# Optimization experiments

Hardware: AMD Instinct MI355X
Metric: run time of the kernel (lower is better)

## Reference

```python
import jax, jax.numpy as jnp
import numpy as np
from jax.scipy.special import logsumexp

NUM_JOINT_TYPES = 17
SINKHORN_ITERS = 30
SINKHORN_TAU = 0.05
BIG_COST = 1.0e6


def _scot_forward(embeddings, W1, b1, prototype_pool, joint_types, k):
    n = embeddings.shape[0]
    # node encoder: Linear + SELU
    h = jax.nn.selu(embeddings @ W1 + b1)  # [N, H]
    prototypes = prototype_pool[:k]        # [K, H] (k <= k_max)
    # squared euclidean distance (torch.cdist(p=2).pow(2))
    d2 = (jnp.sum(h * h, axis=1)[:, None]
          + jnp.sum(prototypes * prototypes, axis=1)[None, :]
          - 2.0 * (h @ prototypes.T))
    d2 = jnp.maximum(d2, 0.0)              # [N, K]
    # expand each person slot to 17 joint-type slots
    cost = jnp.repeat(d2, NUM_JOINT_TYPES, axis=1)          # [N, K*17]
    slot_types = jnp.tile(jnp.arange(NUM_JOINT_TYPES), k)   # [K*17]
    type_mask = joint_types[:, None] == slot_types[None, :]  # [N, K*17]
    cost = jnp.where(type_mask, cost, BIG_COST)

    n_slots = k * NUM_JOINT_TYPES
    log_K = -cost / SINKHORN_TAU
    log_K_ext = jnp.concatenate([log_K, jnp.zeros((n, 1), log_K.dtype)], axis=1)  # [N, K*17+1]
    # target marginal: 1 per slot, slack column absorbs leftover mass
    tm = jnp.ones(n_slots + 1, log_K.dtype).at[-1].set(float(max(n - n_slots, 1)))
    log_tm = jnp.log(tm)

    def step(carry, _):
        log_u, log_v = carry
        log_u = -logsumexp(log_K_ext + log_v[None, :], axis=1)   # row normalization
        log_v = log_tm - logsumexp(log_K_ext + log_u[:, None], axis=0)  # col normalization
        return (log_u, log_v), None

    init = (jnp.zeros(n, log_K.dtype), jnp.zeros(n_slots + 1, log_K.dtype))
    (log_u, log_v), _ = jax.lax.scan(step, init, None, length=SINKHORN_ITERS)

    T = jnp.exp(log_K_ext + log_u[:, None] + log_v[None, :])[:, :n_slots]  # [N, K*17]
    logits = jnp.log(T.reshape(n, k, NUM_JOINT_TYPES).sum(axis=2) + 1e-8)  # [N, K]
    return logits, T


def setup_inputs() -> dict:
    key = jax.random.key(0)
    k_emb, k_w, k_proto, k_jt = jax.random.split(key, 4)
    N, D, H, KMAX = 6144, 256, 256, 512
    emb = jax.random.normal(k_emb, (N, D), dtype=jnp.float32)
    emb = emb / jnp.linalg.norm(emb, axis=1, keepdims=True)  # L2-normalised per docstring
    W1 = jax.random.normal(k_w, (D, H), dtype=jnp.float32) * (1.0 / np.sqrt(D))
    b1 = jnp.zeros((H,), jnp.float32)
    prototype_pool = jax.random.normal(k_proto, (KMAX, H), dtype=jnp.float32) * 0.5
    joint_types = jax.random.randint(k_jt, (N,), 0, NUM_JOINT_TYPES)
    return {"embeddings": emb, "W1": W1, "b1": b1,
            "prototype_pool": prototype_pool, "joint_types": joint_types, "k": 300}


def reference(embeddings, W1, b1, prototype_pool, joint_types, k):
    return _scot_forward(embeddings, W1, b1, prototype_pool, joint_types, k)
```

## Files before the change

kernel.cpp:

```cpp
#include <hip/hip_runtime.h>
#include <math.h>

#define NT 17
#define NBLK 34
#define KCAP 300
#define KP 320
#define LROW 656
#define LCAP 200
#define CH 2
#define NITER 30
#define NCHKMAX 512
#define MSCALE2 28.853900817779268f

typedef unsigned long long u64;
typedef float vfloat4 __attribute__((ext_vector_type(4)));

#define EX2(x) __builtin_amdgcn_exp2f(x)
#define LG2(x) __builtin_amdgcn_logf(x)
#if __has_builtin(__builtin_amdgcn_rcpf)
#define RCP(x) __builtin_amdgcn_rcpf(x)
#else
#define RCP(x) (1.0f / (x))
#endif

__device__ inline unsigned bf16rne(float x) {
  unsigned u = __float_as_uint(x);
  return (u + 0x7FFFu + ((u >> 16) & 1u)) >> 16;
}
__device__ inline unsigned bfp(float lo, float hi) {
  return bf16rne(lo) | (bf16rne(hi) << 16);
}
#define BFLO(p) __uint_as_float((p) << 16)
#define BFHI(p) __uint_as_float((p) & 0xFFFF0000u)


__device__ inline float selu_f(float x) {
  const float scale = 1.0507009873554804934193349852946f;
  const float alpha = 1.6732632423543772848170429916717f;
  return x > 0.f ? scale * x : scale * alpha * (EX2(x * 1.4426950408889634f) - 1.f);
}

__global__ __launch_bounds__(1024) void k_bucket(const int* __restrict__ jt, int n,
    int* __restrict__ meta, int* __restrict__ perm, int* __restrict__ tys,
    unsigned* __restrict__ cmE, unsigned* __restrict__ pcE,
    unsigned* __restrict__ suE) {
  __shared__ int cnt[NCHKMAX][NT];
  __shared__ int tot[NT];
  __shared__ int off[NT];
  int tid = threadIdx.x, lane = tid & 63, wv = tid >> 6;
  int nchk = (n + 63) >> 6;

  for (int i = tid; i < NBLK * 16; i += 1024) cmE[i] = 0u;
  for (int i = tid; i < 4 * NBLK * 16; i += 1024) { pcE[i] = 0u; suE[i] = 0u; }

  for (int ci = wv; ci < nchk; ci += 16) {
    int idx = ci * 64 + lane;
    bool ok = idx < n;
    int t = ok ? jt[idx] : -1;
#pragma unroll
    for (int tt = 0; tt < NT; tt++) {
      u64 b = __ballot(t == tt);
      if (lane == tt) cnt[ci][tt] = (int)__popcll(b);
    }
  }
  __syncthreads();
  if (tid < NT) {
    int run = 0;
    for (int ci = 0; ci < nchk; ci++) {
      int x = cnt[ci][tid];
      cnt[ci][tid] = run;
      run += x;
    }
    tot[tid] = run;
  }
  __syncthreads();
  if (tid == 0) {
    int o = 0;
    for (int t = 0; t < NT; t++) {
      off[t] = o; meta[32 + t] = o; meta[t] = tot[t]; o += tot[t];
    }
  }
  __syncthreads();
  if (tid < NT) {
    int o = off[tid];
    for (int ci = 0; ci < nchk; ci++) cnt[ci][tid] += o;
  }
  __syncthreads();
  for (int ci = wv; ci < nchk; ci += 16) {
    int idx = ci * 64 + lane;
    bool ok = idx < n;
    int t = ok ? jt[idx] : -1;
    u64 myb = 0;
#pragma unroll
    for (int tt = 0; tt < NT; tt++) {
      u64 b = __ballot(t == tt);
      if (t == tt) myb = b;
    }
    if (ok) {
      int rank = (int)__popcll(myb & ((1ull << lane) - 1ull));
      int pos = cnt[ci][t] + rank;
      perm[pos] = idx;
      tys[pos] = t;
    }
  }
}

__global__ __launch_bounds__(256) void k_hgemm(const float* __restrict__ A,
    const float* __restrict__ B, const float* __restrict__ bias,
    float* __restrict__ C, int n, int D, int H) {
  __shared__ __align__(16) float As[16][68];
  __shared__ __align__(16) float Bs[16][68];
  int tid = threadIdx.x;
  int i0 = blockIdx.x * 64, j0 = blockIdx.y * 64;
  int tx = tid & 15, ty = tid >> 4;
  int aI = tid & 63, aK = (tid >> 6) << 2;
  int bJ = (tid & 15) << 2, bK = tid >> 4;
  float acc[4][4] = {};
  for (int k0 = 0; k0 < D; k0 += 16) {
    float4 av = *(const float4*)(A + (size_t)(i0 + aI) * D + k0 + aK);
    float4 bv = *(const float4*)(B + (size_t)(k0 + bK) * H + j0 + bJ);
    __syncthreads();
    As[aK + 0][aI] = av.x; As[aK + 1][aI] = av.y; As[aK + 2][aI] = av.z; As[aK + 3][aI] = av.w;
    *(float4*)(&Bs[bK][bJ]) = bv;
    __syncthreads();
#pragma unroll
    for (int kk = 0; kk < 16; kk++) {
      float4 a4 = *(float4*)(&As[kk][ty << 2]);
      float4 b4 = *(float4*)(&Bs[kk][tx << 2]);
      float aa[4] = {a4.x, a4.y, a4.z, a4.w};
      float bb[4] = {b4.x, b4.y, b4.z, b4.w};
#pragma unroll
      for (int p = 0; p < 4; p++)
#pragma unroll
        for (int q = 0; q < 4; q++)
          acc[p][q] = fmaf(aa[p], bb[q], acc[p][q]);
    }
  }
#pragma unroll
  for (int p = 0; p < 4; p++) {
    int i = i0 + (ty << 2) + p;
    float o[4];
#pragma unroll
    for (int q = 0; q < 4; q++) {
      int j = j0 + (tx << 2) + q;
      o[q] = selu_f(acc[p][q] + bias[j]);
    }
    *(float4*)(C + (size_t)i * H + j0 + (tx << 2)) = make_float4(o[0], o[1], o[2], o[3]);
  }
}

__global__ __launch_bounds__(256) void k_msort(const float* __restrict__ h,
    const float* __restrict__ P, const int* __restrict__ perm,
    float* __restrict__ Ms, int n, int H, int k) {
  __shared__ __align__(16) float As[16][68];
  __shared__ __align__(16) float Bs[16][68];
  __shared__ float hp[4][64];
  __shared__ float pp[4][64];
  __shared__ int gIdx[64];
  int tid = threadIdx.x;
  int i0 = blockIdx.x * 64, j0 = blockIdx.y * 64;
  if (tid < 64) gIdx[tid] = perm[i0 + tid];
  __syncthreads();
  int tx = tid & 15, ty = tid >> 4;
  int aI = tid & 63, aK = (tid >> 6) << 2;
  int gA = gIdx[aI];
  bool bok = (j0 + aI) < k;
  const float* bRow = P + (size_t)(j0 + (bok ? aI : 0)) * H;
  float acc[4][4] = {};
  float ha = 0.f, pa = 0.f;
  for (int k0 = 0; k0 < H; k0 += 16) {
    float4 av = *(const float4*)(h + (size_t)gA * H + k0 + aK);
    float4 bv = *(const float4*)(bRow + k0 + aK);
    ha += av.x * av.x + av.y * av.y + av.z * av.z + av.w * av.w;
    pa += bv.x * bv.x + bv.y * bv.y + bv.z * bv.z + bv.w * bv.w;
    __syncthreads();
    As[aK + 0][aI] = av.x; As[aK + 1][aI] = av.y; As[aK + 2][aI] = av.z; As[aK + 3][aI] = av.w;
    Bs[aK + 0][aI] = bv.x; Bs[aK + 1][aI] = bv.y; Bs[aK + 2][aI] = bv.z; Bs[aK + 3][aI] = bv.w;
    __syncthreads();
#pragma unroll
    for (int kk = 0; kk < 16; kk++) {
      float4 a4 = *(float4*)(&As[kk][ty << 2]);
      float4 b4 = *(float4*)(&Bs[kk][tx << 2]);
      float aa[4] = {a4.x, a4.y, a4.z, a4.w};
      float bb[4] = {b4.x, b4.y, b4.z, b4.w};
#pragma unroll
      for (int p = 0; p < 4; p++)
#pragma unroll
        for (int q = 0; q < 4; q++)
          acc[p][q] = fmaf(aa[p], bb[q], acc[p][q]);
    }
  }
  int grp = tid >> 6;
  hp[grp][aI] = ha;
  pp[grp][aI] = pa;
  __syncthreads();
#pragma unroll
  for (int p = 0; p < 4; p++) {
    int rr = (ty << 2) + p;
    int r = i0 + rr;
    float hq = hp[0][rr] + hp[1][rr] + hp[2][rr] + hp[3][rr];
#pragma unroll
    for (int q = 0; q < 4; q++) {
      int jl = (tx << 2) + q;
      int j = j0 + jl;
      if (j < k) {
        float pq = pp[0][jl] + pp[1][jl] + pp[2][jl] + pp[3][jl];
        float d2 = hq + pq - 2.f * acc[p][q];
        d2 = fmaxf(d2, 0.f);
        Ms[(size_t)r * k + j] = -d2 * MSCALE2;
      }
    }
  }
}

__global__ __launch_bounds__(1024) void k_sink(const float* __restrict__ Ms,
    unsigned short* __restrict__ Ms2, const int* __restrict__ meta,
    float* __restrict__ cmD, unsigned* __restrict__ cmE,
    float* __restrict__ pcD, unsigned* __restrict__ pcE,
    float* __restrict__ suD, unsigned* __restrict__ suE,
    float* __restrict__ uF, float* __restrict__ vF,
    int k, float tm_last) {
  __shared__ __align__(16) char Klds[LCAP * LROW];
  __shared__ __align__(16) float WP2[16][KP];
  __shared__ __align__(16) float V[KP];
  __shared__ __align__(16) float Sown[KP];
  __shared__ float SU[16];
  __shared__ float w_sh;
  __shared__ int lvl_ep;
  __shared__ int pairflag;
  int tid = threadIdx.x, lane = tid & 63, wv = tid >> 6;
  int c = blockIdx.x;
  int t, hb, prt;
  if (c < 32) { t = c & 15; hb = c >> 4; prt = c ^ 16; }
  else        { t = 16;     hb = c & 1;  prt = c ^ 1;  }
  int cRt = meta[t];
  int s0t = meta[32 + t];
  int h0 = (cRt + 1) >> 1;
  int rb = hb ? h0 : 0;
  int re = hb ? cRt : h0;
  int myR = re - rb;
  int s0 = s0t + rb;
  int ntH = (myR + 3) >> 2;
  bool l2v = (lane + 64) < (k >> 2);
  int g = lane >> 4, cg = lane & 15;
  bool r2a = (cg < 8);

  if (tid == 0) { w_sh = 1.f; lvl_ep = 0; pairflag = 0; }

  {
    float4 cm0 = make_float4(-3e38f, -3e38f, -3e38f, -3e38f);
    float4 cm1 = cm0;
    for (int tile = wv; tile < ntH; tile += 16) {
      int r0 = tile * 4;
#pragma unroll
      for (int rr = 0; rr < 4; rr++) {
        int rc = (r0 + rr < myR) ? (r0 + rr) : r0;
        const float4* rp = (const float4*)(Ms + (size_t)(s0 + rc) * k);
        float4 a0 = rp[lane];
        cm0.x = fmaxf(cm0.x, a0.x); cm0.y = fmaxf(cm0.y, a0.y);
        cm0.z = fmaxf(cm0.z, a0.z); cm0.w = fmaxf(cm0.w, a0.w);
        if (l2v) {
          float4 a1 = rp[lane + 64];
          cm1.x = fmaxf(cm1.x, a1.x); cm1.y = fmaxf(cm1.y, a1.y);
          cm1.z = fmaxf(cm1.z, a1.z); cm1.w = fmaxf(cm1.w, a1.w);
        }
      }
    }
    *(float4*)&WP2[wv][4 * lane] = cm0;
    if (l2v) *(float4*)&WP2[wv][4 * (lane + 64)] = cm1;
    __syncthreads();
    if (tid < k) {
      float cmax = WP2[0][tid];
#pragma unroll
      for (int q = 1; q < 16; q++) cmax = fmaxf(cmax, WP2[q][tid]);
      Sown[tid] = cmax;
      __hip_atomic_store(&cmD[c * KP + tid], cmax,
                         __ATOMIC_RELAXED, __HIP_MEMORY_SCOPE_AGENT);
    }
    __syncthreads();
    if (tid == 0) {
      __hip_atomic_store(&cmE[c * 16], 1u, __ATOMIC_RELAXED, __HIP_MEMORY_SCOPE_AGENT);
      while (__hip_atomic_load(&cmE[prt * 16], __ATOMIC_RELAXED, __HIP_MEMORY_SCOPE_AGENT) < 1u)
        __builtin_amdgcn_s_sleep(1);
      __hip_atomic_store(&pairflag, 1, __ATOMIC_RELEASE, __HIP_MEMORY_SCOPE_WORKGROUP);
    }
    if (tid < k) {
      while (__hip_atomic_load(&pairflag, __ATOMIC_ACQUIRE, __HIP_MEMORY_SCOPE_WORKGROUP) < 1)
        __builtin_amdgcn_s_sleep(1);
      float o = __hip_atomic_load(&cmD[prt * KP + tid],
                                  __ATOMIC_RELAXED, __HIP_MEMORY_SCOPE_AGENT);
      V[tid] = fmaxf(Sown[tid], o);
    }
    __syncthreads();
    float4 cx0 = *(const float4*)&V[4 * lane];
    float4 cx1 = l2v ? *(const float4*)&V[4 * (lane + 64)] : cx0;
    for (int tile = wv; tile < ntH; tile += 16) {
      int r0 = tile * 4;
#pragma unroll
      for (int rr = 0; rr < 4; rr++) {
        int r = r0 + rr;
        if (r < myR) {
          const float4* rp = (const float4*)(Ms + (size_t)(s0 + r) * k);
          char* orow = (char*)Ms2 + (size_t)(s0 + r) * (KP * 2);
          char* lrow = Klds + (size_t)r * LROW;
          bool inL = (r < LCAP);
          float4 a0 = rp[lane];
          uint2 o;
          o.x = bfp(EX2(a0.x - cx0.x), EX2(a0.y - cx0.y));
          o.y = bfp(EX2(a0.z - cx0.z), EX2(a0.w - cx0.w));
          *(uint2*)(orow + 8 * lane) = o;
          if (inL) *(uint2*)(lrow + 8 * lane) = o;
          if (l2v) {
            float4 a1 = rp[lane + 64];
            uint2 o1;
            o1.x = bfp(EX2(a1.x - cx1.x), EX2(a1.y - cx1.y));
            o1.y = bfp(EX2(a1.z - cx1.z), EX2(a1.w - cx1.w));
            *(uint2*)(orow + 512 + 8 * lane) = o1;
            if (inL) *(uint2*)(lrow + 512 + 8 * lane) = o1;
          } else if (lane < 16) {
            *(uint2*)(orow + 512 + 8 * lane) = make_uint2(0u, 0u);
            if (inL) *(uint2*)(lrow + 512 + 8 * lane) = make_uint2(0u, 0u);
          }
        }
      }
    }
  }
  __syncthreads();
  if (tid < KP) V[tid] = 0.f;
  __syncthreads();

  for (int m = 0; m < NITER; m++) {
    int epoch = m + 1;
    int slot = m & 3;
    if (wv == 15) {
      if (m > 0) {
        int pslot = (m - 1) & 3;
        unsigned want = (unsigned)m;
        bool need = lane < NBLK;
        for (;;) {
          bool ok = !need ||
              (__hip_atomic_load(&suE[(pslot * NBLK + lane) * 16],
                                 __ATOMIC_RELAXED, __HIP_MEMORY_SCOPE_AGENT) >= want);
          if (__all(ok)) break;
          __builtin_amdgcn_s_sleep(1);
        }
        float s = need
            ? __hip_atomic_load(&suD[(pslot * NBLK + lane) * 16],
                                __ATOMIC_RELAXED, __HIP_MEMORY_SCOPE_AGENT)
            : 0.f;
#pragma unroll
        for (int o = 32; o; o >>= 1) s += __shfl_xor(s, o);
        if (lane == 0) w_sh = tm_last / s;
      }
      if (lane == 0)
        __hip_atomic_store(&lvl_ep, epoch, __ATOMIC_RELEASE, __HIP_MEMORY_SCOPE_WORKGROUP);
    }
    float w = 0.f;
    bool haveW = (wv == 15);
    float su = 0.f;
    float vv[3][8];
#pragma unroll
    for (int q3 = 0; q3 < 3; q3++) {
      if (q3 < 2 || r2a) {
        float4 x0 = *(const float4*)&V[q3 * 128 + cg * 8];
        float4 x1 = *(const float4*)&V[q3 * 128 + cg * 8 + 4];
        vv[q3][0] = x0.x; vv[q3][1] = x0.y; vv[q3][2] = x0.z; vv[q3][3] = x0.w;
        vv[q3][4] = x1.x; vv[q3][5] = x1.y; vv[q3][6] = x1.z; vv[q3][7] = x1.w;
      } else {
#pragma unroll
        for (int e = 0; e < 8; e++) vv[q3][e] = 0.f;
      }
    }
    float acc[3][8];
#pragma unroll
    for (int q3 = 0; q3 < 3; q3++)
#pragma unroll
      for (int e = 0; e < 8; e++) acc[q3][e] = 0.f;

    int t0 = (wv < 15) ? wv : ntH;
    for (; t0 < ntH; t0 += 15 * CH) {
      uint4 T[CH][3];
      float rs[CH];
#pragma unroll
      for (int ccc = 0; ccc < CH; ccc++) {
        int tile = t0 + 15 * ccc;
        rs[ccc] = 0.f;
        if (tile < ntH) {
          int r = tile * 4 + g;
          int rc = (r < myR) ? r : (myR - 1);
          uint4 z4 = make_uint4(0u, 0u, 0u, 0u);
          if (rc < LCAP) {
            const uint4* lp = (const uint4*)(Klds + (size_t)rc * LROW + (cg << 4));
            T[ccc][0] = lp[0];
            T[ccc][1] = lp[16];
            if (r2a) T[ccc][2] = lp[32]; else T[ccc][2] = z4;
          } else {
            const uint4* gp = (const uint4*)((const char*)Ms2 +
                (size_t)(s0 + rc) * (KP * 2) + (cg << 4));
            T[ccc][0] = gp[0];
            T[ccc][1] = gp[16];
            if (r2a) T[ccc][2] = gp[32]; else T[ccc][2] = z4;
          }
          float r1 = 0.f;
#pragma unroll
          for (int q3 = 0; q3 < 3; q3++) {
            r1 = fmaf(BFLO(T[ccc][q3].x), vv[q3][0], r1);
            r1 = fmaf(BFHI(T[ccc][q3].x), vv[q3][1], r1);
            r1 = fmaf(BFLO(T[ccc][q3].y), vv[q3][2], r1);
            r1 = fmaf(BFHI(T[ccc][q3].y), vv[q3][3], r1);
            r1 = fmaf(BFLO(T[ccc][q3].z), vv[q3][4], r1);
            r1 = fmaf(BFHI(T[ccc][q3].z), vv[q3][5], r1);
            r1 = fmaf(BFLO(T[ccc][q3].w), vv[q3][6], r1);
            r1 = fmaf(BFHI(T[ccc][q3].w), vv[q3][7], r1);
          }
          r1 += __shfl_xor(r1, 1); r1 += __shfl_xor(r1, 2);
          r1 += __shfl_xor(r1, 4); r1 += __shfl_xor(r1, 8);
          rs[ccc] = r1;
        }
      }
      if (!haveW) {
        while (__hip_atomic_load(&lvl_ep, __ATOMIC_ACQUIRE, __HIP_MEMORY_SCOPE_WORKGROUP) < epoch)
          __builtin_amdgcn_s_sleep(1);
        w = w_sh;
        haveW = true;
      }
#pragma unroll
      for (int ccc = 0; ccc < CH; ccc++) {
        int tile = t0 + 15 * ccc;
        if (tile < ntH) {
          int r = tile * 4 + g;
          bool valid = (r < myR);
          float u = RCP(rs[ccc] + w);
          float uu = valid ? u : 0.f;
          if (cg == 0) {
            su += uu;
            if (valid && m == NITER - 1) uF[s0 + r] = u;
          }
#pragma unroll
          for (int q3 = 0; q3 < 3; q3++) {
            acc[q3][0] = fmaf(BFLO(T[ccc][q3].x), uu, acc[q3][0]);
            acc[q3][1] = fmaf(BFHI(T[ccc][q3].x), uu, acc[q3][1]);
            acc[q3][2] = fmaf(BFLO(T[ccc][q3].y), uu, acc[q3][2]);
            acc[q3][3] = fmaf(BFHI(T[ccc][q3].y), uu, acc[q3][3]);
            acc[q3][4] = fmaf(BFLO(T[ccc][q3].z), uu, acc[q3][4]);
            acc[q3][5] = fmaf(BFHI(T[ccc][q3].z), uu, acc[q3][5]);
            acc[q3][6] = fmaf(BFLO(T[ccc][q3].w), uu, acc[q3][6]);
            acc[q3][7] = fmaf(BFHI(T[ccc][q3].w), uu, acc[q3][7]);
          }
        }
      }
    }
    if (!haveW) {
      while (__hip_atomic_load(&lvl_ep, __ATOMIC_ACQUIRE, __HIP_MEMORY_SCOPE_WORKGROUP) < epoch)
        __builtin_amdgcn_s_sleep(1);
      haveW = true;
    }

    if (wv < 15) {
#pragma unroll
      for (int q3 = 0; q3 < 3; q3++)
#pragma unroll
        for (int e = 0; e < 8; e++) {
          float a = acc[q3][e];
          a += __shfl_xor(a, 16);
          a += __shfl_xor(a, 32);
          acc[q3][e] = a;
        }
      if (lane < 16) {
#pragma unroll
        for (int q3 = 0; q3 < 3; q3++) {
          if (q3 < 2 || lane < 8) {
            *(float4*)&WP2[wv][q3 * 128 + lane * 8] =
                make_float4(acc[q3][0], acc[q3][1], acc[q3][2], acc[q3][3]);
            *(float4*)&WP2[wv][q3 * 128 + lane * 8 + 4] =
                make_float4(acc[q3][4], acc[q3][5], acc[q3][6], acc[q3][7]);
          }
        }
      }
      float sr = su;
      sr += __shfl_xor(sr, 16);
      sr += __shfl_xor(sr, 32);
      if (lane == 0) SU[wv] = sr;
    }
    __syncthreads();
    if (tid < k) {
      float s = WP2[0][tid];
#pragma unroll
      for (int q = 1; q < 15; q++) s += WP2[q][tid];
      Sown[tid] = s;
      __hip_atomic_store(&pcD[(slot * NBLK + c) * KP + tid], s,
                         __ATOMIC_RELAXED, __HIP_MEMORY_SCOPE_AGENT);
    }
    if (wv == 15) {
      float sp = (lane < 15) ? SU[lane] : 0.f;
#pragma unroll
      for (int o = 32; o; o >>= 1) sp += __shfl_xor(sp, o);
      if (lane == 0)
        __hip_atomic_store(&suD[(slot * NBLK + c) * 16], sp,
                           __ATOMIC_RELAXED, __HIP_MEMORY_SCOPE_AGENT);
      __builtin_amdgcn_s_waitcnt(0);
      if (lane == 0)
        __hip_atomic_store(&suE[(slot * NBLK + c) * 16], (unsigned)epoch,
                           __ATOMIC_RELAXED, __HIP_MEMORY_SCOPE_AGENT);
    }
    __syncthreads();
    if (tid == 0) {
      __hip_atomic_store(&pcE[(slot * NBLK + c) * 16], (unsigned)epoch,
                         __ATOMIC_RELAXED, __HIP_MEMORY_SCOPE_AGENT);
      while (__hip_atomic_load(&pcE[(slot * NBLK + prt) * 16],
                               __ATOMIC_RELAXED, __HIP_MEMORY_SCOPE_AGENT) < (unsigned)epoch)
        __builtin_amdgcn_s_sleep(1);
      __hip_atomic_store(&pairflag, m + 2, __ATOMIC_RELEASE, __HIP_MEMORY_SCOPE_WORKGROUP);
    }
    if (tid < k) {
      while (__hip_atomic_load(&pairflag, __ATOMIC_ACQUIRE, __HIP_MEMORY_SCOPE_WORKGROUP) < m + 2)
        __builtin_amdgcn_s_sleep(1);
      float sp = __hip_atomic_load(&pcD[(slot * NBLK + prt) * KP + tid],
                                   __ATOMIC_RELAXED, __HIP_MEMORY_SCOPE_AGENT);
      V[tid] = RCP(Sown[tid] + sp);
    }
    __syncthreads();
  }
  if (hb == 0)
    for (int j = tid; j < k; j += 1024) vF[(size_t)t * k + j] = V[j];
}

__global__ __launch_bounds__(256) void k_epi(const unsigned short* __restrict__ Ms2,
    const float* __restrict__ uF, const float* __restrict__ vF,
    const int* __restrict__ perm, const int* __restrict__ tys,
    float* __restrict__ out, int n, int k) {
  __shared__ float vals[KCAP];
  int r = blockIdx.x;
  int i = perm[r], t = tys[r];
  float u = uF[r];
  const unsigned short* Krow = Ms2 + (size_t)r * KP;
  const float* Vrow = vF + (size_t)t * k;
  for (int j = threadIdx.x; j < k; j += 256)
    vals[j] = __uint_as_float((unsigned)Krow[j] << 16) * u * Vrow[j];
  __syncthreads();
  float* lg = out + (size_t)i * k;
  for (int j = threadIdx.x; j < k; j += 256)
    __builtin_nontemporal_store(LG2(vals[j] + 1e-8f) * 0.6931471805599453f, &lg[j]);
  int ns = k * NT;
  float* Trow = out + (size_t)n * k + (size_t)i * ns;
  if ((ns & 3) == 0) {
    int n4 = ns >> 2;
    int o0 = threadIdx.x << 2;
    int rmod = o0 % NT;
    for (int g4 = threadIdx.x; g4 < n4; g4 += 256, o0 += 1024) {
      int sstar = t - rmod; if (sstar < 0) sstar += NT;
      int j = (unsigned)(o0 + sstar) / (unsigned)NT;
      float vv = vals[j < k ? j : 0];
      vfloat4 v;
      v.x = (sstar == 0) ? vv : 0.f;
      v.y = (sstar == 1) ? vv : 0.f;
      v.z = (sstar == 2) ? vv : 0.f;
      v.w = (sstar == 3) ? vv : 0.f;
      __builtin_nontemporal_store(v, (vfloat4*)(Trow + o0));
      rmod += 4; if (rmod >= NT) rmod -= NT;
    }
  } else {
    for (int o = threadIdx.x; o < ns; o += 256) {
      int j = o / NT;
      int tt = o - j * NT;
      Trow[o] = (tt == t) ? vals[j] : 0.f;
    }
  }
}

extern "C" void kernel_launch(void* const* d_in, const int* in_sizes, int n_in,
                              void* d_out, int out_size, void* d_ws, size_t ws_size,
                              hipStream_t stream) {
  const float* emb = (const float*)d_in[0];
  const float* W1  = (const float*)d_in[1];
  const float* b1  = (const float*)d_in[2];
  const float* P   = (const float*)d_in[3];
  const int*   jt  = (const int*)d_in[4];
  (void)n_in; (void)ws_size;

  const int n = in_sizes[4];
  const int H = in_sizes[2];
  const int D = in_sizes[1] / H;
  const int k = out_size / (n * (NT + 1));
  const int nslots = k * NT;
  const float tm_last = (float)((n - nslots) > 1 ? (n - nslots) : 1);

  char* w = (char*)d_ws;
  size_t off = 0;
  auto take = [&](size_t bytes) -> char* {
    char* p = w + off;
    off = (off + bytes + 255) & ~(size_t)255;
    return p;
  };
  int*      meta = (int*)take(4096);
  int*      perm = (int*)take((size_t)n * 4);
  int*      tys  = (int*)take((size_t)n * 4);
  float*    h    = (float*)take((size_t)n * H * 4);
  float*    Ms   = (float*)take((size_t)n * k * 4);
  unsigned short* Ms2 = (unsigned short*)take((size_t)n * KP * 2 + 1024);
  float*    cmD  = (float*)take((size_t)NBLK * KP * 4);
  unsigned* cmE  = (unsigned*)take((size_t)NBLK * 64);
  float*    pcD  = (float*)take((size_t)4 * NBLK * KP * 4);
  unsigned* pcE  = (unsigned*)take((size_t)4 * NBLK * 64);
  float*    suD  = (float*)take((size_t)4 * NBLK * 64);
  unsigned* suE  = (unsigned*)take((size_t)4 * NBLK * 64);
  float*    uF   = (float*)take((size_t)n * 4);
  float*    vF   = (float*)take((size_t)NT * k * 4);

  k_bucket<<<1, 1024, 0, stream>>>(jt, n, meta, perm, tys, cmE, pcE, suE);
  k_hgemm<<<dim3(n / 64, H / 64), dim3(256), 0, stream>>>(emb, W1, b1, h, n, D, H);
  k_msort<<<dim3(n / 64, (k + 63) / 64), dim3(256), 0, stream>>>(h, P, perm, Ms, n, H, k);
  k_sink<<<NBLK, 1024, 0, stream>>>(Ms, Ms2, meta, cmD, cmE, pcD, pcE,
                                    suD, suE, uF, vF, k, tm_last);
  k_epi<<<n, 256, 0, stream>>>(Ms2, uF, vF, perm, tys, (float*)d_out, n, k);
}
```

Before: 422.1 us.

## Replace pair-flag handoff with per-wave direct partner polling in Sinkhorn loop

Removes the shared-memory pairflag relay and the per-iteration tail barrier. Each compute wave now polls the partner block's epoch flag itself and computes column scalings directly from the partner's partial sums at the start of the next iteration, so the per-iteration V write and extra __syncthreads go away. The final vF is computed the same way after the loop. This trades one block-wide barrier per iteration for redundant per-wave global atomic loads and reciprocal work. Sown reuse across iterations could race if not guarded by the existing barriers.

```diff
diff --git a/kernel.cpp b/kernel.cpp
--- a/kernel.cpp
+++ b/kernel.cpp
@@ -227,7 +227,6 @@
   __shared__ float SU[16];
   __shared__ float w_sh;
   __shared__ int lvl_ep;
-  __shared__ int pairflag;
   int tid = threadIdx.x, lane = tid & 63, wv = tid >> 6;
   int c = blockIdx.x;
   int t, hb, prt;
@@ -245,7 +244,7 @@
   int g = lane >> 4, cg = lane & 15;
   bool r2a = (cg < 8);
 
-  if (tid == 0) { w_sh = 1.f; lvl_ep = 0; pairflag = 0; }
+  if (tid == 0) { w_sh = 1.f; lvl_ep = 0; }
 
   {
     float4 cm0 = make_float4(-3e38f, -3e38f, -3e38f, -3e38f);
@@ -278,14 +277,10 @@
                          __ATOMIC_RELAXED, __HIP_MEMORY_SCOPE_AGENT);
     }
     __syncthreads();
-    if (tid == 0) {
-      __hip_atomic_store(&cmE[c * 16], 1u, __ATOMIC_RELAXED, __HIP_MEMORY_SCOPE_AGENT);
-      while (__hip_atomic_load(&cmE[prt * 16], __ATOMIC_RELAXED, __HIP_MEMORY_SCOPE_AGENT) < 1u)
-        __builtin_amdgcn_s_sleep(1);
-      __hip_atomic_store(&pairflag, 1, __ATOMIC_RELEASE, __HIP_MEMORY_SCOPE_WORKGROUP);
-    }
+    if (tid == 0)
+      __hip_atomic_store(&cmE[c * 16], 1u, __ATOMIC_RELEASE, __HIP_MEMORY_SCOPE_AGENT);
     if (tid < k) {
-      while (__hip_atomic_load(&pairflag, __ATOMIC_ACQUIRE, __HIP_MEMORY_SCOPE_WORKGROUP) < 1)
+      while (__hip_atomic_load(&cmE[prt * 16], __ATOMIC_ACQUIRE, __HIP_MEMORY_SCOPE_AGENT) < 1u)
         __builtin_amdgcn_s_sleep(1);
       float o = __hip_atomic_load(&cmD[prt * KP + tid],
                                   __ATOMIC_RELAXED, __HIP_MEMORY_SCOPE_AGENT);
@@ -326,8 +321,6 @@
     }
   }
   __syncthreads();
-  if (tid < KP) V[tid] = 0.f;
-  __syncthreads();
 
   for (int m = 0; m < NITER; m++) {
     int epoch = m + 1;
@@ -360,15 +353,26 @@
     float su = 0.f;
     float vv[3][8];
 #pragma unroll
-    for (int q3 = 0; q3 < 3; q3++) {
-      if (q3 < 2 || r2a) {
-        float4 x0 = *(const float4*)&V[q3 * 128 + cg * 8];
-        float4 x1 = *(const float4*)&V[q3 * 128 + cg * 8 + 4];
-        vv[q3][0] = x0.x; vv[q3][1] = x0.y; vv[q3][2] = x0.z; vv[q3][3] = x0.w;
-        vv[q3][4] = x1.x; vv[q3][5] = x1.y; vv[q3][6] = x1.z; vv[q3][7] = x1.w;
-      } else {
-#pragma unroll
-        for (int e = 0; e < 8; e++) vv[q3][e] = 0.f;
+    for (int q3 = 0; q3 < 3; q3++)
+#pragma unroll
+      for (int e = 0; e < 8; e++) vv[q3][e] = 0.f;
+    if (wv < 15 && m > 0) {
+      int pslot = (m - 1) & 3;
+      while (__hip_atomic_load(&pcE[(pslot * NBLK + prt) * 16],
+                               __ATOMIC_ACQUIRE, __HIP_MEMORY_SCOPE_AGENT) < (unsigned)m)
+        __builtin_amdgcn_s_sleep(1);
+      const float* pd = pcD + ((size_t)pslot * NBLK + prt) * KP;
+#pragma unroll
+      for (int q3 = 0; q3 < 3; q3++) {
+#pragma unroll
+        for (int e = 0; e < 8; e++) {
+          int idx = q3 * 128 + cg * 8 + e;
+          if ((q3 < 2 || r2a) && idx < k) {
+            float sp = __hip_atomic_load(&pd[idx],
+                                         __ATOMIC_RELAXED, __HIP_MEMORY_SCOPE_AGENT);
+            vv[q3][e] = RCP(Sown[idx] + sp);
+          }
+        }
       }
     }
     float acc[3][8];
@@ -484,11 +488,15 @@
     }
     __syncthreads();
     if (tid < k) {
-      float s = WP2[0][tid];
-#pragma unroll
-      for (int q = 1; q < 15; q++) s += WP2[q][tid];
+      float sA = WP2[0][tid];
+#pragma unroll
+      for (int q = 1; q < 8; q++) sA += WP2[q][tid];
+      float sB = WP2[8][tid];
+#pragma unroll
+      for (int q = 9; q < 15; q++) sB += WP2[q][tid];
+      float s = sA + sB;
       Sown[tid] = s;
-      __hip_atomic_store(&pcD[(slot * NBLK + c) * KP + tid], s,
+      __hip_atomic_store(&pcD[((size_t)slot * NBLK + c) * KP + tid], s,
                          __ATOMIC_RELAXED, __HIP_MEMORY_SCOPE_AGENT);
     }
     if (wv == 15) {
@@ -504,25 +512,19 @@
                            __ATOMIC_RELAXED, __HIP_MEMORY_SCOPE_AGENT);
     }
     __syncthreads();
-    if (tid == 0) {
+    if (tid == 0)
       __hip_atomic_store(&pcE[(slot * NBLK + c) * 16], (unsigned)epoch,
-                         __ATOMIC_RELAXED, __HIP_MEMORY_SCOPE_AGENT);
-      while (__hip_atomic_load(&pcE[(slot * NBLK + prt) * 16],
-                               __ATOMIC_RELAXED, __HIP_MEMORY_SCOPE_AGENT) < (unsigned)epoch)
-        __builtin_amdgcn_s_sleep(1);
-      __hip_atomic_store(&pairflag, m + 2, __ATOMIC_RELEASE, __HIP_MEMORY_SCOPE_WORKGROUP);
-    }
-    if (tid < k) {
-      while (__hip_atomic_load(&pairflag, __ATOMIC_ACQUIRE, __HIP_MEMORY_SCOPE_WORKGROUP) < m + 2)
-        __builtin_amdgcn_s_sleep(1);
-      float sp = __hip_atomic_load(&pcD[(slot * NBLK + prt) * KP + tid],
-                                   __ATOMIC_RELAXED, __HIP_MEMORY_SCOPE_AGENT);
-      V[tid] = RCP(Sown[tid] + sp);
-    }
-    __syncthreads();
-  }
-  if (hb == 0)
-    for (int j = tid; j < k; j += 1024) vF[(size_t)t * k + j] = V[j];
+                         __ATOMIC_RELEASE, __HIP_MEMORY_SCOPE_AGENT);
+  }
+  if (hb == 0 && tid < k) {
+    int fslot = (NITER - 1) & 3;
+    while (__hip_atomic_load(&pcE[(fslot * NBLK + prt) * 16],
+                             __ATOMIC_ACQUIRE, __HIP_MEMORY_SCOPE_AGENT) < (unsigned)NITER)
+      __builtin_amdgcn_s_sleep(1);
+    float sp = __hip_atomic_load(&pcD[((size_t)fslot * NBLK + prt) * KP + tid],
+                                 __ATOMIC_RELAXED, __HIP_MEMORY_SCOPE_AGENT);
+    vF[(size_t)t * k + tid] = RCP(Sown[tid] + sp);
+  }
 }
 
 __global__ __launch_bounds__(256) void k_epi(const unsigned short* __restrict__ Ms2,
```

Result: slower. 785.7 us (+86.2%).
